# Kernel optimization log

Measured on AMD Instinct MI355X. Metric: run time of the kernel, lower is better.

The kernel has to match this reference:

```python
import jax, jax.numpy as jnp
import numpy as np
from jax import lax

B, T, C_IN, C_OUT, H = 2048, 128, 2, 16, 232


def setup_inputs() -> dict:
    key = jax.random.key(0)
    k0, k1, k2, k3 = jax.random.split(key, 4)
    X = jax.random.normal(k0, (B, T, C_IN), dtype=jnp.float32)
    # kaiming_normal init (fan_in mode) as in reset_parameters
    conv_w = jax.random.normal(k1, (C_OUT, C_IN, 3), dtype=jnp.float32) * np.sqrt(2.0 / (C_IN * 3))
    conv_b = jnp.zeros((C_OUT,), dtype=jnp.float32)
    w_ih = jax.random.normal(k2, (3 * H, C_OUT), dtype=jnp.float32) * np.sqrt(2.0 / C_OUT)
    w_hh = jax.random.normal(k3, (3 * H, H), dtype=jnp.float32) * np.sqrt(2.0 / H)
    b_ih = jnp.zeros((3 * H,), dtype=jnp.float32)
    b_hh = jnp.zeros((3 * H,), dtype=jnp.float32)
    return {"X": X, "conv_w": conv_w, "conv_b": conv_b,
            "w_ih": w_ih, "w_hh": w_hh, "b_ih": b_ih, "b_hh": b_hh}


def reference(X, conv_w, conv_b, w_ih, w_hh, b_ih, b_hh):
    # Conv1d(2->16, k=3, pad=1) on [B, C, T] + ReLU
    Xc = jnp.transpose(X, (0, 2, 1))                      # [B, 2, T]
    y = lax.conv_general_dilated(Xc, conv_w, window_strides=(1,),
                                 padding=[(1, 1)],
                                 dimension_numbers=("NCH", "OIH", "NCH"))
    y = jax.nn.relu(y + conv_b[None, :, None])            # [B, 16, T]
    x_embed = jnp.transpose(y, (0, 2, 1))                 # [B, T, 16]

    # GRU (torch gate order: r, z, n). Precompute input projections for all t.
    gi = jnp.einsum("btc,gc->btg", x_embed, w_ih) + b_ih  # [B, T, 3H]

    def step(h, g_t):
        gh = h @ w_hh.T + b_hh                            # [B, 3H]
        ir, iz, in_ = jnp.split(g_t, 3, axis=-1)
        hr, hz, hn = jnp.split(gh, 3, axis=-1)
        r = jax.nn.sigmoid(ir + hr)
        z = jax.nn.sigmoid(iz + hz)
        n = jnp.tanh(in_ + r * hn)
        h_new = (1.0 - z) * n + z * h
        return h_new, None

    h0 = jnp.zeros((X.shape[0], w_hh.shape[1]), dtype=X.dtype)
    hT, _ = lax.scan(step, h0, jnp.moveaxis(gi, 1, 0))    # final state [B, H]
    return hT
```

## Files before the change

kernel.cpp:

```cpp
#include <hip/hip_runtime.h>

#define BATCH 2048
#define T     128
#define CIN   2
#define COUT  16
#define H     232
#define RPB   8
#define NBLK  (BATCH/RPB)
#define NTHR  512
#define NGRP  15
#define NT2   48
#define NS    9
#define HROW  272
#define HBUF_H (RPB * HROW)

#define OFF_HA   0
#define SZ_HA    (2 * RPB * HROW * 2)
#define OFF_XE   (OFF_HA + SZ_HA)
#define SZ_XE    (T * RPB * 16 * 2)
#define OFF_WL   (OFF_XE + SZ_XE)
#define SZ_WL    (8 * 14 * 64 * 8 * 2)
#define OFF_CW   (OFF_WL + SZ_WL)
#define SZ_CW    512
#define SMEM_BYTES (OFF_CW + SZ_CW)
#define OFF_XE_H (OFF_XE / 2)

#define L2E   1.4426950408889634f
#define TWO_L2E 2.8853900817779268f

typedef _Float16 half8 __attribute__((ext_vector_type(8)));
typedef float  floatx4 __attribute__((ext_vector_type(4)));

#define MFMA __builtin_amdgcn_mfma_f32_16x16x32_f16
#define SBAR0() __builtin_amdgcn_sched_barrier(0)

__device__ __align__(16) _Float16 g_packedW[NT2 * NS * 64 * 8];

__global__ void pack_w_kernel(const float* __restrict__ w_ih,
                              const float* __restrict__ w_hh) {
  int tile = blockIdx.x, slice = blockIdx.y, lane = threadIdx.x;
  int grp = tile / NGRP;
  int j   = (tile % NGRP) * 16 + (lane & 15);
  int g   = grp * H + j;
  bool valid = (tile < 3 * NGRP) && (j < H);
  half8 v = {};
  if (valid) {
#pragma unroll
    for (int i = 0; i < 8; ++i) {
      int k = slice * 32 + ((lane >> 4) << 3) + i;
      float f = 0.f;
      if (slice < 8) {
        if (k < H) f = w_hh[g * H + k];
        else if (k < H + COUT && grp < 2) f = w_ih[g * COUT + (k - H)];
      } else {
        int xk = k - 256;
        if (xk >= 0 && xk < COUT && grp == 2) f = w_ih[g * COUT + xk];
      }
      v[i] = (_Float16)f;
    }
  }
  *(half8*)&g_packedW[((tile * NS + slice) * 64 + lane) * 8] = v;
}

__global__ __launch_bounds__(NTHR, 2) void st_gru_kernel(
    const float* __restrict__ X,
    const float* __restrict__ conv_w, const float* __restrict__ conv_b,
    const float* __restrict__ b_ih, const float* __restrict__ b_hh,
    float* __restrict__ out) {

  extern __shared__ __align__(16) char smem[];
  _Float16* lds16  = (_Float16*)smem;
  _Float16* hAflat = (_Float16*)(smem + OFF_HA);
  _Float16* Xemb   = (_Float16*)(smem + OFF_XE);
  _Float16* wLDS   = (_Float16*)(smem + OFF_WL);
  float*    cwp    = (float*)(smem + OFF_CW);

  const int tid  = threadIdx.x;
  const int lane = tid & 63;
  const int wave = tid >> 6;
  const int r_a  = lane & 15;
  const int ch4  = lane >> 4;
  const int blk  = blockIdx.x;
  const int rr   = r_a & 7;
  const int swz  = rr & 3;

  for (int i = tid; i < 2 * RPB * HROW; i += NTHR) hAflat[i] = (_Float16)0;
  if (tid < COUT * CIN * 3) cwp[tid] = conv_w[tid];
  if (tid < COUT) cwp[96 + tid] = conv_b[tid];
  __syncthreads();

  for (int p = tid; p < RPB * T; p += NTHR) {
    int r = p >> 7, t = p & (T - 1);
    const float* xr = X + (size_t)(blk * RPB + r) * (T * CIN);
    float x0[3], x1[3];
#pragma unroll
    for (int d = 0; d < 3; ++d) {
      int tt = t + d - 1;
      bool ok = (unsigned)tt < (unsigned)T;
      x0[d] = ok ? xr[tt * 2] : 0.f;
      x1[d] = ok ? xr[tt * 2 + 1] : 0.f;
    }
    half8 lo, hi;
#pragma unroll
    for (int c = 0; c < COUT; ++c) {
      float a = cwp[96 + c];
#pragma unroll
      for (int d = 0; d < 3; ++d)
        a += x0[d] * cwp[c * 6 + d] + x1[d] * cwp[c * 6 + 3 + d];
      _Float16 hv = (_Float16)fmaxf(a, 0.f);
      if (c < 8) lo[c] = hv; else hi[c - 8] = hv;
    }
    *(half8*)&Xemb[(t * RPB + r) * 16] = lo;
    *(half8*)&Xemb[(t * RPB + r) * 16 + 8] = hi;
  }

  const int gi0 = wave * 2, gi1 = wave * 2 + 1;
  const bool g1ok = (gi1 < NGRP);
  const int tr0 = gi0, tz0 = gi0 + NGRP, tn0 = gi0 + 2 * NGRP;
  const int tr1 = g1ok ? gi1 : 45, tz1 = g1ok ? gi1 + NGRP : 46, tn1 = g1ok ? gi1 + 2 * NGRP : 47;
  const half8* Wp = (const half8*)g_packedW;

  half8* myz = (half8*)(wLDS + wave * (14 * 64 * 8));
#pragma unroll
  for (int f = 0; f < 6; ++f) myz[f * 64 + lane] = Wp[(tz0 * NS + f) * 64 + lane];
#pragma unroll
  for (int f = 0; f < 6; ++f) myz[(6 + f) * 64 + lane] = Wp[(tz1 * NS + f) * 64 + lane];
  myz[12 * 64 + lane] = Wp[(tn0 * NS + 8) * 64 + lane];
  myz[13 * 64 + lane] = Wp[(tn1 * NS + 8) * 64 + lane];

  half8 wr0[8], wr1[8], wn0[8], wn1[8], wzh0[2], wzh1[2];
#pragma unroll
  for (int s = 0; s < 8; ++s) {
    wr0[s] = Wp[(tr0 * NS + s) * 64 + lane];
    wr1[s] = Wp[(tr1 * NS + s) * 64 + lane];
    wn0[s] = Wp[(tn0 * NS + s) * 64 + lane];
    wn1[s] = Wp[(tn1 * NS + s) * 64 + lane];
  }
  wzh0[0] = Wp[(tz0 * NS + 6) * 64 + lane];
  wzh0[1] = Wp[(tz0 * NS + 7) * 64 + lane];
  wzh1[0] = Wp[(tz1 * NS + 6) * 64 + lane];
  wzh1[1] = Wp[(tz1 * NS + 7) * 64 + lane];

  const int j0 = gi0 * 16 + r_a, j1 = gi1 * 16 + r_a;
  float nbsr0 = 0.f, nbsz0 = 0.f, bin0 = 0.f, bhn0 = 0.f;
  float nbsr1 = 0.f, nbsz1 = 0.f, bin1 = 0.f, bhn1 = 0.f;
  if (j0 < H) {
    nbsr0 = -L2E * (b_ih[j0] + b_hh[j0]);
    nbsz0 = -L2E * (b_ih[H + j0] + b_hh[H + j0]);
    bin0 = b_ih[2 * H + j0]; bhn0 = b_hh[2 * H + j0];
  }
  if (g1ok && j1 < H) {
    nbsr1 = -L2E * (b_ih[j1] + b_hh[j1]);
    nbsz1 = -L2E * (b_ih[H + j1] + b_hh[H + j1]);
    bin1 = b_ih[2 * H + j1]; bhn1 = b_hh[2 * H + j1];
  }

  const int eb   = (ch4 & 2);
  const int rowb = ((ch4 & 1) << 2) | (ch4 & 2);

  int woff0[2], woff1[2];
#pragma unroll
  for (int u = 0; u < 2; ++u) {
    int row = rowb + u;
    woff0[u] = row * HROW + ((j0 & ~31) | ((((j0 >> 3) & 3) ^ (row & 3)) << 3) | (j0 & 7));
    woff1[u] = row * HROW + ((j1 & ~31) | ((((j1 >> 3) & 3) ^ (row & 3)) << 3) | (j1 & 7));
  }

  float h0[2] = {0.f, 0.f};
  float h1[2] = {0.f, 0.f};

  const int aoff = rr * HROW + ((ch4 ^ swz) << 3);
  const int inc7 = (ch4 == 0) ? 0 : 256;
  int pa7_e = (ch4 == 0) ? (0      + rr * HROW + 224 + (swz << 3))
                         : (OFF_XE_H + rr * 16 + ((ch4 == 2) ? 8 : 0));
  int pa7_o = (ch4 == 0) ? (HBUF_H + rr * HROW + 224 + (swz << 3))
                         : (OFF_XE_H + 128 + rr * 16 + ((ch4 == 2) ? 8 : 0));
  int a8i = OFF_XE_H + rr * 16 + ((ch4 & 1) << 3);

  __syncthreads();

#define GRU_STEP(RBH, WBH, PA7, A8I) do {                                      \
    half8 A_[7];                                                               \
    _Pragma("unroll")                                                          \
    for (int s = 0; s < 7; ++s)                                                \
      A_[s] = *(const half8*)&lds16[(RBH) + aoff + s * 32];                    \
    half8 A7_ = *(const half8*)&lds16[(PA7)];                                  \
    half8 A8_ = *(const half8*)&lds16[(A8I)];                                  \
      \
    floatx4 ra0 = {}, na0 = {}, za0 = {}, ra1 = {}, na1 = {}, za1 = {};        \
    _Pragma("unroll")                                                          \
    for (int s = 0; s < 7; ++s) {                                              \
      ra0 = MFMA(A_[s], wr0[s], ra0, 0, 0, 0);                                 \
      na0 = MFMA(A_[s], wn0[s], na0, 0, 0, 0);                                 \
      if (g1ok) {                                                              \
        ra1 = MFMA(A_[s], wr1[s], ra1, 0, 0, 0);                               \
        na1 = MFMA(A_[s], wn1[s], na1, 0, 0, 0);                               \
      }                                                                        \
    }                                                                          \
    za0 = MFMA(A_[6], wzh0[0], za0, 0, 0, 0);                                  \
    za0 = MFMA(A7_, wzh0[1], za0, 0, 0, 0);                                    \
    ra0 = MFMA(A7_, wr0[7], ra0, 0, 0, 0);                                     \
    na0 = MFMA(A7_, wn0[7], na0, 0, 0, 0);                                     \
    if (g1ok) {                                                                \
      za1 = MFMA(A_[6], wzh1[0], za1, 0, 0, 0);                                \
      za1 = MFMA(A7_, wzh1[1], za1, 0, 0, 0);                                  \
      ra1 = MFMA(A7_, wr1[7], ra1, 0, 0, 0);                                   \
      na1 = MFMA(A7_, wn1[7], na1, 0, 0, 0);                                   \
    }                                                                          \
       \
    float sr0_[2], sr1_[2];                                                    \
    _Pragma("unroll")                                                          \
    for (int u = 0; u < 2; ++u) {                                              \
      sr0_[u] = __builtin_amdgcn_rcpf(                                         \
          1.f + __builtin_amdgcn_exp2f(fmaf(ra0[eb + u], -L2E, nbsr0)));       \
      sr1_[u] = __builtin_amdgcn_rcpf(                                         \
          1.f + __builtin_amdgcn_exp2f(fmaf(ra1[eb + u], -L2E, nbsr1)));       \
    }                                                                          \
    SBAR0();                                                                   \
                        \
    floatx4 xa0 = {};                                                          \
    _Pragma("unroll")                                                          \
    for (int s = 0; s < 6; ++s)                                                \
      za0 = MFMA(A_[s], myz[s * 64 + lane], za0, 0, 0, 0);                     \
    xa0 = MFMA(A8_, myz[12 * 64 + lane], xa0, 0, 0, 0);                        \
                                   \
    _Pragma("unroll")                                                          \
    for (int u = 0; u < 2; ++u) {                                              \
      float sz = __builtin_amdgcn_rcpf(                                        \
          1.f + __builtin_amdgcn_exp2f(fmaf(za0[eb + u], -L2E, nbsz0)));       \
      float pre = fmaf(sr0_[u], na0[eb + u] + bhn0, xa0[eb + u] + bin0);       \
      float e2 = __builtin_amdgcn_exp2f(pre * TWO_L2E);                        \
      float n = fmaf(-2.f, __builtin_amdgcn_rcpf(e2 + 1.f), 1.f);              \
      h0[u] = fmaf(sz, h0[u] - n, n);                                          \
      lds16[(WBH) + woff0[u]] = (_Float16)h0[u];                               \
    }                                                                          \
    SBAR0();                                                                   \
                        \
    if (g1ok) {                                                                \
      floatx4 xa1 = {};                                                        \
      _Pragma("unroll")                                                        \
      for (int s = 0; s < 6; ++s)                                              \
        za1 = MFMA(A_[s], myz[(6 + s) * 64 + lane], za1, 0, 0, 0);             \
      xa1 = MFMA(A8_, myz[13 * 64 + lane], xa1, 0, 0, 0);                      \
                                          \
      _Pragma("unroll")                                                        \
      for (int u = 0; u < 2; ++u) {                                            \
        float sz = __builtin_amdgcn_rcpf(                                      \
            1.f + __builtin_amdgcn_exp2f(fmaf(za1[eb + u], -L2E, nbsz1)));     \
        float pre = fmaf(sr1_[u], na1[eb + u] + bhn1, xa1[eb + u] + bin1);     \
        float e2 = __builtin_amdgcn_exp2f(pre * TWO_L2E);                      \
        float n = fmaf(-2.f, __builtin_amdgcn_rcpf(e2 + 1.f), 1.f);            \
        h1[u] = fmaf(sz, h1[u] - n, n);                                        \
        lds16[(WBH) + woff1[u]] = (_Float16)h1[u];                             \
      }                                                                        \
    }                                                                          \
    __syncthreads();                                                           \
  } while (0)

  for (int tt = 0; tt < T; tt += 2) {
    GRU_STEP(0,      HBUF_H, pa7_e, a8i);
    GRU_STEP(HBUF_H, 0,      pa7_o, a8i + 128);
    pa7_e += inc7; pa7_o += inc7; a8i += 256;
  }
#undef GRU_STEP

#pragma unroll
  for (int u = 0; u < 2; ++u) {
    int row = rowb + u;
    if (j0 < H) out[(size_t)(blk * RPB + row) * H + j0] = h0[u];
    if (g1ok && j1 < H) out[(size_t)(blk * RPB + row) * H + j1] = h1[u];
  }
}

extern "C" void kernel_launch(void* const* d_in, const int* in_sizes, int n_in,
                              void* d_out, int out_size, void* d_ws, size_t ws_size,
                              hipStream_t stream) {
  const float* X      = (const float*)d_in[0];
  const float* conv_w = (const float*)d_in[1];
  const float* conv_b = (const float*)d_in[2];
  const float* w_ih   = (const float*)d_in[3];
  const float* w_hh   = (const float*)d_in[4];
  const float* b_ih   = (const float*)d_in[5];
  const float* b_hh   = (const float*)d_in[6];
  float* out = (float*)d_out;

  static bool attr_set = false;
  if (!attr_set) {
    hipFuncSetAttribute((const void*)st_gru_kernel,
                        hipFuncAttributeMaxDynamicSharedMemorySize, SMEM_BYTES);
    attr_set = true;
  }

  pack_w_kernel<<<dim3(NT2, NS), 64, 0, stream>>>(w_ih, w_hh);
  st_gru_kernel<<<NBLK, NTHR, SMEM_BYTES, stream>>>(X, conv_w, conv_b, b_ih, b_hh, out);
}
```

Baseline: 195.9 us.

## Rebalance z-gate weights between registers and LDS and interleave gate MFMAs

Moves two more z-gate weight slices per tile from LDS into registers, shrinking the per-wave LDS weight region, and preloads the remaining LDS z weights at the start of each step. The step is restructured so the second tile's MFMAs are interleaved with the first tile's sigmoid and tanh math instead of being separated by scheduling barriers. The g1ok guards are removed, so the last wave always computes its dummy second tile. The intent is to hide transcendental latency behind matrix work, at the cost of higher register pressure and the wasted dummy-tile work.

```diff
diff --git a/kernel.cpp b/kernel.cpp
--- a/kernel.cpp
+++ b/kernel.cpp
@@ -19,20 +19,19 @@
 #define OFF_XE   (OFF_HA + SZ_HA)
 #define SZ_XE    (T * RPB * 16 * 2)
 #define OFF_WL   (OFF_XE + SZ_XE)
-#define SZ_WL    (8 * 14 * 64 * 8 * 2)
+#define SZ_WL    (8 * 10 * 64 * 8 * 2)
 #define OFF_CW   (OFF_WL + SZ_WL)
 #define SZ_CW    512
 #define SMEM_BYTES (OFF_CW + SZ_CW)
 #define OFF_XE_H (OFF_XE / 2)
 
-#define L2E   1.4426950408889634f
+#define L2E     1.4426950408889634f
 #define TWO_L2E 2.8853900817779268f
 
 typedef _Float16 half8 __attribute__((ext_vector_type(8)));
 typedef float  floatx4 __attribute__((ext_vector_type(4)));
 
 #define MFMA __builtin_amdgcn_mfma_f32_16x16x32_f16
-#define SBAR0() __builtin_amdgcn_sched_barrier(0)
 
 __device__ __align__(16) _Float16 g_packedW[NT2 * NS * 64 * 8];
 
@@ -120,15 +119,15 @@
   const int tr1 = g1ok ? gi1 : 45, tz1 = g1ok ? gi1 + NGRP : 46, tn1 = g1ok ? gi1 + 2 * NGRP : 47;
   const half8* Wp = (const half8*)g_packedW;
 
-  half8* myz = (half8*)(wLDS + wave * (14 * 64 * 8));
-#pragma unroll
-  for (int f = 0; f < 6; ++f) myz[f * 64 + lane] = Wp[(tz0 * NS + f) * 64 + lane];
-#pragma unroll
-  for (int f = 0; f < 6; ++f) myz[(6 + f) * 64 + lane] = Wp[(tz1 * NS + f) * 64 + lane];
-  myz[12 * 64 + lane] = Wp[(tn0 * NS + 8) * 64 + lane];
-  myz[13 * 64 + lane] = Wp[(tn1 * NS + 8) * 64 + lane];
-
-  half8 wr0[8], wr1[8], wn0[8], wn1[8], wzh0[2], wzh1[2];
+  half8* myz = (half8*)(wLDS + wave * (10 * 64 * 8));
+#pragma unroll
+  for (int f = 0; f < 4; ++f) myz[f * 64 + lane] = Wp[(tz0 * NS + f) * 64 + lane];
+#pragma unroll
+  for (int f = 0; f < 4; ++f) myz[(4 + f) * 64 + lane] = Wp[(tz1 * NS + f) * 64 + lane];
+  myz[8 * 64 + lane] = Wp[(tn0 * NS + 8) * 64 + lane];
+  myz[9 * 64 + lane] = Wp[(tn1 * NS + 8) * 64 + lane];
+
+  half8 wr0[8], wr1[8], wn0[8], wn1[8], wzh0[4], wzh1[4];
 #pragma unroll
   for (int s = 0; s < 8; ++s) {
     wr0[s] = Wp[(tr0 * NS + s) * 64 + lane];
@@ -136,10 +135,11 @@
     wn0[s] = Wp[(tn0 * NS + s) * 64 + lane];
     wn1[s] = Wp[(tn1 * NS + s) * 64 + lane];
   }
-  wzh0[0] = Wp[(tz0 * NS + 6) * 64 + lane];
-  wzh0[1] = Wp[(tz0 * NS + 7) * 64 + lane];
-  wzh1[0] = Wp[(tz1 * NS + 6) * 64 + lane];
-  wzh1[1] = Wp[(tz1 * NS + 7) * 64 + lane];
+#pragma unroll
+  for (int s = 0; s < 4; ++s) {
+    wzh0[s] = Wp[(tz0 * NS + 4 + s) * 64 + lane];
+    wzh1[s] = Wp[(tz1 * NS + 4 + s) * 64 + lane];
+  }
 
   const int j0 = gi0 * 16 + r_a, j1 = gi1 * 16 + r_a;
   float nbsr0 = 0.f, nbsz0 = 0.f, bin0 = 0.f, bhn0 = 0.f;
@@ -180,79 +180,87 @@
   __syncthreads();
 
 #define GRU_STEP(RBH, WBH, PA7, A8I) do {                                      \
+                     \
     half8 A_[7];                                                               \
     _Pragma("unroll")                                                          \
     for (int s = 0; s < 7; ++s)                                                \
       A_[s] = *(const half8*)&lds16[(RBH) + aoff + s * 32];                    \
     half8 A7_ = *(const half8*)&lds16[(PA7)];                                  \
     half8 A8_ = *(const half8*)&lds16[(A8I)];                                  \
-      \
-    floatx4 ra0 = {}, na0 = {}, za0 = {}, ra1 = {}, na1 = {}, za1 = {};        \
-    _Pragma("unroll")                                                          \
-    for (int s = 0; s < 7; ++s) {                                              \
+    half8 zf0_[4], zf1_[4], xf0_, xf1_;                                        \
+    _Pragma("unroll")                                                          \
+    for (int s = 0; s < 4; ++s) {                                              \
+      zf0_[s] = myz[s * 64 + lane];                                            \
+      zf1_[s] = myz[(4 + s) * 64 + lane];                                      \
+    }                                                                          \
+    xf0_ = myz[8 * 64 + lane];                                                 \
+    xf1_ = myz[9 * 64 + lane];                                                 \
+                           \
+    floatx4 ra0 = {}, za0 = {}, na0 = {}, xa0 = {};                            \
+    _Pragma("unroll")                                                          \
+    for (int s = 0; s < 4; ++s) {                                              \
       ra0 = MFMA(A_[s], wr0[s], ra0, 0, 0, 0);                                 \
+      za0 = MFMA(A_[s], zf0_[s], za0, 0, 0, 0);                                \
       na0 = MFMA(A_[s], wn0[s], na0, 0, 0, 0);                                 \
-      if (g1ok) {                                                              \
-        ra1 = MFMA(A_[s], wr1[s], ra1, 0, 0, 0);                               \
-        na1 = MFMA(A_[s], wn1[s], na1, 0, 0, 0);                               \
-      }                                                                        \
-    }                                                                          \
-    za0 = MFMA(A_[6], wzh0[0], za0, 0, 0, 0);                                  \
-    za0 = MFMA(A7_, wzh0[1], za0, 0, 0, 0);                                    \
+    }                                                                          \
+    _Pragma("unroll")                                                          \
+    for (int s = 4; s < 7; ++s) {                                              \
+      ra0 = MFMA(A_[s], wr0[s], ra0, 0, 0, 0);                                 \
+      za0 = MFMA(A_[s], wzh0[s - 4], za0, 0, 0, 0);                            \
+      na0 = MFMA(A_[s], wn0[s], na0, 0, 0, 0);                                 \
+    }                                                                          \
     ra0 = MFMA(A7_, wr0[7], ra0, 0, 0, 0);                                     \
+    za0 = MFMA(A7_, wzh0[3], za0, 0, 0, 0);                                    \
     na0 = MFMA(A7_, wn0[7], na0, 0, 0, 0);                                     \
-    if (g1ok) {                                                                \
-      za1 = MFMA(A_[6], wzh1[0], za1, 0, 0, 0);                                \
-      za1 = MFMA(A7_, wzh1[1], za1, 0, 0, 0);                                  \
-      ra1 = MFMA(A7_, wr1[7], ra1, 0, 0, 0);                                   \
-      na1 = MFMA(A7_, wn1[7], na1, 0, 0, 0);                                   \
-    }                                                                          \
-       \
-    float sr0_[2], sr1_[2];                                                    \
+    xa0 = MFMA(A8_, xf0_, xa0, 0, 0, 0);                                       \
+                                       \
+    floatx4 ra1 = {}, za1 = {}, na1 = {}, xa1 = {};                            \
+    _Pragma("unroll")                                                          \
+    for (int s = 0; s < 4; ++s) {                                              \
+      ra1 = MFMA(A_[s], wr1[s], ra1, 0, 0, 0);                                 \
+      za1 = MFMA(A_[s], zf1_[s], za1, 0, 0, 0);                                \
+      na1 = MFMA(A_[s], wn1[s], na1, 0, 0, 0);                                 \
+    }                                                                          \
+                      \
+    float sr_[2], sz_[2];                                                      \
     _Pragma("unroll")                                                          \
     for (int u = 0; u < 2; ++u) {                                              \
-      sr0_[u] = __builtin_amdgcn_rcpf(                                         \
+      sr_[u] = __builtin_amdgcn_rcpf(                                          \
           1.f + __builtin_amdgcn_exp2f(fmaf(ra0[eb + u], -L2E, nbsr0)));       \
-      sr1_[u] = __builtin_amdgcn_rcpf(                                         \
-          1.f + __builtin_amdgcn_exp2f(fmaf(ra1[eb + u], -L2E, nbsr1)));       \
-    }                                                                          \
-    SBAR0();                                                                   \
-                        \
-    floatx4 xa0 = {};                                                          \
-    _Pragma("unroll")                                                          \
-    for (int s = 0; s < 6; ++s)                                                \
-      za0 = MFMA(A_[s], myz[s * 64 + lane], za0, 0, 0, 0);                     \
-    xa0 = MFMA(A8_, myz[12 * 64 + lane], xa0, 0, 0, 0);                        \
-                                   \
+      sz_[u] = __builtin_amdgcn_rcpf(                                          \
+          1.f + __builtin_amdgcn_exp2f(fmaf(za0[eb + u], -L2E, nbsz0)));       \
+    }                                                                          \
+    _Pragma("unroll")                                                          \
+    for (int s = 4; s < 7; ++s) {                                              \
+      ra1 = MFMA(A_[s], wr1[s], ra1, 0, 0, 0);                                 \
+      za1 = MFMA(A_[s], wzh1[s - 4], za1, 0, 0, 0);                            \
+      na1 = MFMA(A_[s], wn1[s], na1, 0, 0, 0);                                 \
+    }                                                                          \
+                                        \
     _Pragma("unroll")                                                          \
     for (int u = 0; u < 2; ++u) {                                              \
-      float sz = __builtin_amdgcn_rcpf(                                        \
-          1.f + __builtin_amdgcn_exp2f(fmaf(za0[eb + u], -L2E, nbsz0)));       \
-      float pre = fmaf(sr0_[u], na0[eb + u] + bhn0, xa0[eb + u] + bin0);       \
+      float pre = fmaf(sr_[u], na0[eb + u] + bhn0, xa0[eb + u] + bin0);        \
       float e2 = __builtin_amdgcn_exp2f(pre * TWO_L2E);                        \
       float n = fmaf(-2.f, __builtin_amdgcn_rcpf(e2 + 1.f), 1.f);              \
-      h0[u] = fmaf(sz, h0[u] - n, n);                                          \
+      h0[u] = fmaf(sz_[u], h0[u] - n, n);                                      \
       lds16[(WBH) + woff0[u]] = (_Float16)h0[u];                               \
     }                                                                          \
-    SBAR0();                                                                   \
-                        \
-    if (g1ok) {                                                                \
-      floatx4 xa1 = {};                                                        \
-      _Pragma("unroll")                                                        \
-      for (int s = 0; s < 6; ++s)                                              \
-        za1 = MFMA(A_[s], myz[(6 + s) * 64 + lane], za1, 0, 0, 0);             \
-      xa1 = MFMA(A8_, myz[13 * 64 + lane], xa1, 0, 0, 0);                      \
-                                          \
-      _Pragma("unroll")                                                        \
-      for (int u = 0; u < 2; ++u) {                                            \
-        float sz = __builtin_amdgcn_rcpf(                                      \
-            1.f + __builtin_amdgcn_exp2f(fmaf(za1[eb + u], -L2E, nbsz1)));     \
-        float pre = fmaf(sr1_[u], na1[eb + u] + bhn1, xa1[eb + u] + bin1);     \
-        float e2 = __builtin_amdgcn_exp2f(pre * TWO_L2E);                      \
-        float n = fmaf(-2.f, __builtin_amdgcn_rcpf(e2 + 1.f), 1.f);            \
-        h1[u] = fmaf(sz, h1[u] - n, n);                                        \
-        lds16[(WBH) + woff1[u]] = (_Float16)h1[u];                             \
-      }                                                                        \
+    ra1 = MFMA(A7_, wr1[7], ra1, 0, 0, 0);                                     \
+    za1 = MFMA(A7_, wzh1[3], za1, 0, 0, 0);                                    \
+    na1 = MFMA(A7_, wn1[7], na1, 0, 0, 0);                                     \
+    xa1 = MFMA(A8_, xf1_, xa1, 0, 0, 0);                                       \
+                                                                 \
+    _Pragma("unroll")                                                          \
+    for (int u = 0; u < 2; ++u) {                                              \
+      float r = __builtin_amdgcn_rcpf(                                         \
+          1.f + __builtin_amdgcn_exp2f(fmaf(ra1[eb + u], -L2E, nbsr1)));       \
+      float z = __builtin_amdgcn_rcpf(                                         \
+          1.f + __builtin_amdgcn_exp2f(fmaf(za1[eb + u], -L2E, nbsz1)));       \
+      float pre = fmaf(r, na1[eb + u] + bhn1, xa1[eb + u] + bin1);             \
+      float e2 = __builtin_amdgcn_exp2f(pre * TWO_L2E);                        \
+      float n = fmaf(-2.f, __builtin_amdgcn_rcpf(e2 + 1.f), 1.f);              \
+      h1[u] = fmaf(z, h1[u] - n, n);                                           \
+      lds16[(WBH) + woff1[u]] = (_Float16)h1[u];   \
     }                                                                          \
     __syncthreads();                                                           \
   } while (0)
```

Result: faster. 177.9 us (-9.2%).
